# Optimization experiments

Measured on AMD Instinct MI355X. Metric: run time of the kernel, lower is better.

The kernel has to match this reference:

```python
import jax, jax.numpy as jnp
import numpy as np

FORGET_BIAS = 1.0  # TF BasicLSTMCell default

def _lstm_cell(c, h, x, W, b):
    # TF BasicLSTMCell: concat([x, h]) @ W + b, split into i, j(=g), f, o
    z = jnp.concatenate([x, h], axis=-1) @ W + b
    i, j, f, o = jnp.split(z, 4, axis=-1)
    c_new = c * jax.nn.sigmoid(f + FORGET_BIAS) + jax.nn.sigmoid(i) * jnp.tanh(j)
    h_new = jnp.tanh(c_new) * jax.nn.sigmoid(o)
    return c_new, h_new

def setup_inputs() -> dict:
    V, B, T, U = 16000, 64, 128, 256
    key = jax.random.key(0)
    ks = jax.random.split(key, 6)
    s_in = 1.0 / np.sqrt(2 * U)
    return {
        "input_data": jax.random.randint(ks[0], (B, T), 0, V, dtype=jnp.int32),
        "targets": jax.random.randint(ks[1], (B, T), 0, V, dtype=jnp.int32),
        "embedding": jax.random.normal(ks[2], (V, U), dtype=jnp.float32) * 0.1,
        "W0": jax.random.normal(ks[3], (2 * U, 4 * U), dtype=jnp.float32) * s_in,
        "b0": jnp.zeros((4 * U,), dtype=jnp.float32),
        "W1": jax.random.normal(ks[4], (2 * U, 4 * U), dtype=jnp.float32) * s_in,
        "b1": jnp.zeros((4 * U,), dtype=jnp.float32),
        "softmax_w": jax.random.normal(ks[5], (U, V), dtype=jnp.float32) * (1.0 / np.sqrt(U)),
        "softmax_b": jnp.zeros((V,), dtype=jnp.float32),
    }

def reference(input_data, targets, embedding, W0, b0, W1, b1, softmax_w, softmax_b):
    B, T = input_data.shape
    U = embedding.shape[1]
    # embedding lookup -> [B, T, U], scan over time (time-major)
    xs = embedding[input_data].transpose(1, 0, 2)  # [T, B, U]
    zeros = jnp.zeros((B, U), dtype=embedding.dtype)

    def step(carry, x):
        c0, h0, c1, h1 = carry
        c0, h0 = _lstm_cell(c0, h0, x, W0, b0)
        c1, h1 = _lstm_cell(c1, h1, h0, W1, b1)
        return (c0, h0, c1, h1), h1

    _, outs = jax.lax.scan(step, (zeros, zeros, zeros, zeros), xs)  # [T, B, U]
    output = outs.transpose(1, 0, 2).reshape(B * T, U)
    logits = output @ softmax_w + softmax_b  # [B*T, V]
    logp = jax.nn.log_softmax(logits, axis=-1)
    tgt = targets.reshape(-1)
    nll = -jnp.take_along_axis(logp, tgt[:, None], axis=-1)[:, 0]
    cost = jnp.sum(nll) / (B * T)
    return cost
```

## Files before the change

### kernel.cpp

```cpp
#include <hip/hip_runtime.h>
#include <hip/hip_bf16.h>
#include <stdint.h>

typedef __attribute__((ext_vector_type(8))) short short8;
typedef __attribute__((ext_vector_type(4))) float f32x4;
typedef unsigned long long u64;

#define DI static __device__ __forceinline__

DI unsigned short f2b(float f){
  unsigned u = __float_as_uint(f);
  u = (u + 0x7FFFu + ((u >> 16) & 1u)) >> 16;
  return (unsigned short)u;
}
DI float sigm(float x){ return 1.0f / (1.0f + __expf(-x)); }
DI float tanh_(float x){ return 1.0f - 2.0f / (__expf(2.0f*x) + 1.0f); }

__global__ void k_gather(const int* __restrict__ inp, const float* __restrict__ emb,
                         unsigned short* __restrict__ Xbf){
  int r = blockIdx.x;
  int t = r >> 6, b = r & 63;
  int idx = inp[b*128 + t];
  float v = emb[(size_t)idx*256 + threadIdx.x];
  Xbf[(size_t)r*256 + threadIdx.x] = f2b(v);
}

template<int BF, int REORD>
__global__ void k_transpose(const float* __restrict__ src, void* __restrict__ dst,
                            int R, int C, int ld, int row0){
  __shared__ float tile[32][33];
  int tx = threadIdx.x, ty = threadIdx.y;
  int x = blockIdx.x*32 + tx;
  for (int i = 0; i < 4; i++){
    int y = blockIdx.y*32 + ty + i*8;
    if (x < C && y < R) tile[ty + i*8][tx] = src[(size_t)(row0 + y)*ld + x];
  }
  __syncthreads();
  int y2 = blockIdx.y*32 + tx;
  for (int i = 0; i < 4; i++){
    int x2 = blockIdx.x*32 + ty + i*8;
    if (x2 < C && y2 < R){
      float v = tile[tx][ty + i*8];
      int n = REORD ? ((x2 & 255)*4 + (x2 >> 2 >> 6)) : x2;
      if (BF) ((unsigned short*)dst)[(size_t)n*R + y2] = f2b(v);
      else    ((float*)dst)[(size_t)n*R + y2] = v;
    }
  }
}

template<int EPI>
__launch_bounds__(256, 2)
__global__ void k_gemm(const unsigned short* __restrict__ A, const unsigned short* __restrict__ Bt,
                       float* __restrict__ outZ, const float* __restrict__ bias,
                       const int* __restrict__ tgt, float* __restrict__ S, float* __restrict__ LT){
  __shared__ unsigned short As[128*64];
  __shared__ unsigned short Bs[128*64];
  __shared__ int tgt_s[128];
  const int m0 = blockIdx.y*128, n0 = blockIdx.x*128;
  const int tid = threadIdx.x;
  const int w = tid >> 6, l = tid & 63;
  const int quad = l >> 4, l15 = l & 15;
  const int wm = (w >> 1)*64, wn = (w & 1)*64;
  const int lrow = l >> 3, ls = l & 7;
  f32x4 acc[4][4] = {};
  if (EPI == 1 && tid < 128) tgt_s[tid] = tgt[m0 + tid];

  for (int k0 = 0; k0 < 256; k0 += 64){
    #pragma unroll
    for (int it = 0; it < 4; it++){
      int row = it*32 + w*8 + lrow;
      int csrc = ls ^ (row & 7);
      __builtin_amdgcn_global_load_lds(
        (const __attribute__((address_space(1))) unsigned*)&A[(size_t)(m0+row)*256 + k0 + csrc*8],
        (__attribute__((address_space(3))) unsigned*)&As[(it*32 + w*8)*64], 16, 0, 0);
      __builtin_amdgcn_global_load_lds(
        (const __attribute__((address_space(1))) unsigned*)&Bt[(size_t)(n0+row)*256 + k0 + csrc*8],
        (__attribute__((address_space(3))) unsigned*)&Bs[(it*32 + w*8)*64], 16, 0, 0);
    }
    __syncthreads();
    #pragma unroll
    for (int ks = 0; ks < 64; ks += 32){
      const int cki = (ks >> 3) + quad;
      short8 af[4], bfr[4];
      #pragma unroll
      for (int i = 0; i < 4; i++){
        int row = wm + i*16 + l15;
        af[i]  = *(short8*)&As[row*64 + (cki ^ (row & 7))*8];
      }
      #pragma unroll
      for (int j = 0; j < 4; j++){
        int row = wn + j*16 + l15;
        bfr[j] = *(short8*)&Bs[row*64 + (cki ^ (row & 7))*8];
      }
      #pragma unroll
      for (int i = 0; i < 4; i++)
        #pragma unroll
        for (int j = 0; j < 4; j++)
          acc[i][j] = __builtin_amdgcn_mfma_f32_16x16x32_bf16(af[i], bfr[j], acc[i][j], 0, 0, 0);
    }
    __syncthreads();
  }

  if (EPI == 0){
    #pragma unroll
    for (int i = 0; i < 4; i++){
      int mg = m0 + wm + i*16 + quad*4;
      int t = mg >> 6, b = mg & 63;
      #pragma unroll
      for (int j = 0; j < 4; j++){
        int ng = n0 + wn + j*16 + l15;
        float bb = bias[(ng & 3)*256 + (ng >> 2)];
        f32x4 v = acc[i][j];
        v[0] += bb; v[1] += bb; v[2] += bb; v[3] += bb;
        *(f32x4*)&outZ[((size_t)t*1024 + ng)*64 + b] = v;
      }
    }
  } else {
    #pragma unroll
    for (int i = 0; i < 4; i++){
      float rs[4] = {0.f,0.f,0.f,0.f};
      #pragma unroll
      for (int j = 0; j < 4; j++){
        int ng = n0 + wn + j*16 + l15;
        float bb = bias[ng];
        f32x4 v = acc[i][j];
        #pragma unroll
        for (int r = 0; r < 4; r++){
          float e = v[r] + bb;
          int mloc = wm + i*16 + quad*4 + r;
          if (tgt_s[mloc] == ng) LT[m0 + mloc] = e;
          rs[r] += __expf(e);
        }
      }
      #pragma unroll
      for (int r = 0; r < 4; r++){
        float s = rs[r];
        s += __shfl_xor(s, 1, 16);
        s += __shfl_xor(s, 2, 16);
        s += __shfl_xor(s, 4, 16);
        s += __shfl_xor(s, 8, 16);
        if (l15 == 0) atomicAdd(&S[m0 + wm + i*16 + quad*4 + r], s);
      }
    }
  }
}

DI void stage32(const u64* __restrict__ src, unsigned* __restrict__ dst4, int tid, unsigned tagexp){
  u64 v[32];
  for (;;){
    bool ok = true;
    #pragma unroll
    for (int k = 0; k < 32; k++)
      v[k] = __hip_atomic_load(src + tid + k*256, __ATOMIC_RELAXED, __HIP_MEMORY_SCOPE_AGENT);
    #pragma unroll
    for (int k = 0; k < 32; k++)
      ok &= ((unsigned)(v[k] >> 32) == tagexp);
    if (ok) break;
    __builtin_amdgcn_s_sleep(1);
  }
  #pragma unroll
  for (int k = 0; k < 32; k++)
    dst4[tid + k*256] = (unsigned)v[k];
}

__launch_bounds__(256, 1)
__global__ void k_lstm(const float* __restrict__ Z0x,
                       const unsigned short* __restrict__ W0h,
                       const unsigned short* __restrict__ W1,
                       const float* __restrict__ b1,
                       u64* __restrict__ h0h,
                       u64* __restrict__ h1h,
                       unsigned short* __restrict__ H1bf){
  __shared__ __align__(16) char smraw[65536];
  unsigned short* hs = (unsigned short*)smraw;
  unsigned* hs4 = (unsigned*)smraw;
  float* zl = (float*)smraw;

  const int wg = blockIdx.x;
  const bool L0 = (wg < 8);
  const int tid = threadIdx.x;
  const int w = tid >> 6, l = tid & 63, quad = l >> 4, l15 = l & 15;
  const int b = tid & 63;

  short8 bw[16];
  float c_st[8];
  float b1r[16];
  #pragma unroll
  for (int i = 0; i < 8; i++) c_st[i] = 0.f;

  if (L0){
    const int n0 = wg*128;
    #pragma unroll
    for (int j = 0; j < 2; j++)
      #pragma unroll
      for (int ks = 0; ks < 8; ks++)
        bw[j*8+ks] = *(const short8*)&W0h[(size_t)(n0 + w*32 + j*16 + l15)*256 + ks*32 + quad*8];
  } else {
    const int n0 = (wg-8)*64;
    #pragma unroll
    for (int ks = 0; ks < 16; ks++)
      bw[ks] = *(const short8*)&W1[(size_t)(n0 + w*16 + l15)*512 + ks*32 + quad*8];
    const int u0 = (wg-8)*16, ul0 = w*4;
    #pragma unroll
    for (int ul = 0; ul < 4; ul++)
      #pragma unroll
      for (int g = 0; g < 4; g++)
        b1r[ul*4+g] = b1[g*256 + u0 + ul0 + ul];
  }

  if (L0){
    for (int t = 0; t < 128; t++){
      const int n0 = wg*128;
      f32x4 acc[4][2];
      #pragma unroll
      for (int i = 0; i < 4; i++)
        #pragma unroll
        for (int j = 0; j < 2; j++){
          int cl = w*32 + j*16 + l15;
          acc[i][j] = *(const f32x4*)&Z0x[((size_t)t*1024 + n0 + cl)*64 + i*16 + quad*4];
        }
      if (t > 0){
        stage32(h0h + (size_t)(t-1)*8192, hs4, tid, (unsigned)t);
        __syncthreads();
        #pragma unroll
        for (int ks = 0; ks < 8; ks++){
          short8 a[4];
          #pragma unroll
          for (int i = 0; i < 4; i++)
            a[i] = *(const short8*)&hs[(((ks*4+quad)*64) + i*16 + l15)*8];
          #pragma unroll
          for (int i = 0; i < 4; i++)
            #pragma unroll
            for (int j = 0; j < 2; j++)
              acc[i][j] = __builtin_amdgcn_mfma_f32_16x16x32_bf16(a[i], bw[j*8+ks], acc[i][j], 0, 0, 0);
        }
        __syncthreads();
      }
      #pragma unroll
      for (int i = 0; i < 4; i++)
        #pragma unroll
        for (int j = 0; j < 2; j++){
          int cl = w*32 + j*16 + l15;
          *(f32x4*)&zl[cl*68 + i*16 + quad*4] = acc[i][j];
        }
      __syncthreads();
      const int ul0 = w*8;
      unsigned short hout[8];
      #pragma unroll
      for (int ui = 0; ui < 8; ui++){
        int cc = (ul0 + ui)*4;
        float zi = zl[(cc+0)*68 + b], zj = zl[(cc+1)*68 + b];
        float zf = zl[(cc+2)*68 + b], zo = zl[(cc+3)*68 + b];
        float c = c_st[ui]*sigm(zf + 1.0f) + sigm(zi)*tanh_(zj);
        c_st[ui] = c;
        hout[ui] = f2b(tanh_(c)*sigm(zo));
      }
      const size_t base = (size_t)t*8192 + ((size_t)(wg*4 + w)*64 + b)*4;
      #pragma unroll
      for (int j = 0; j < 4; j++){
        u64 val = ((u64)(unsigned)(t+1) << 32)
                | (unsigned)hout[2*j] | ((unsigned)hout[2*j+1] << 16);
        __hip_atomic_store(h0h + base + j, val, __ATOMIC_RELAXED, __HIP_MEMORY_SCOPE_AGENT);
      }
      __syncthreads();
    }
  } else {
    for (int t = 0; t < 128; t++){
      stage32(h0h + (size_t)t*8192, hs4, tid, (unsigned)(t+1));
      __syncthreads();
      f32x4 acc[4];
      #pragma unroll
      for (int i = 0; i < 4; i++) acc[i] = (f32x4){0.f,0.f,0.f,0.f};
      #pragma unroll
      for (int ks = 0; ks < 8; ks++){
        short8 a[4];
        #pragma unroll
        for (int i = 0; i < 4; i++)
          a[i] = *(const short8*)&hs[(((ks*4+quad)*64) + i*16 + l15)*8];
        #pragma unroll
        for (int i = 0; i < 4; i++)
          acc[i] = __builtin_amdgcn_mfma_f32_16x16x32_bf16(a[i], bw[ks], acc[i], 0, 0, 0);
      }
      if (t > 0){
        stage32(h1h + (size_t)(t-1)*8192, hs4 + 8192, tid, (unsigned)t);
        __syncthreads();
        #pragma unroll
        for (int ks = 8; ks < 16; ks++){
          short8 a[4];
          #pragma unroll
          for (int i = 0; i < 4; i++)
            a[i] = *(const short8*)&hs[(((ks*4+quad)*64) + i*16 + l15)*8];
          #pragma unroll
          for (int i = 0; i < 4; i++)
            acc[i] = __builtin_amdgcn_mfma_f32_16x16x32_bf16(a[i], bw[ks], acc[i], 0, 0, 0);
        }
      }
      __syncthreads();
      {
        int cl = w*16 + l15;
        #pragma unroll
        for (int i = 0; i < 4; i++)
          *(f32x4*)&zl[cl*68 + i*16 + quad*4] = acc[i];
      }
      __syncthreads();
      const int u0 = (wg-8)*16, ul0 = w*4;
      unsigned short hout[4];
      #pragma unroll
      for (int ui = 0; ui < 4; ui++){
        int cc = (ul0 + ui)*4;
        float zi = zl[(cc+0)*68 + b] + b1r[ui*4+0];
        float zj = zl[(cc+1)*68 + b] + b1r[ui*4+1];
        float zf = zl[(cc+2)*68 + b] + b1r[ui*4+2];
        float zo = zl[(cc+3)*68 + b] + b1r[ui*4+3];
        float c = c_st[ui]*sigm(zf + 1.0f) + sigm(zi)*tanh_(zj);
        c_st[ui] = c;
        hout[ui] = f2b(tanh_(c)*sigm(zo));
      }
      const int u = u0 + ul0;
      const size_t base = (size_t)t*8192 + ((size_t)(u >> 3)*64 + b)*4 + ((u & 4) >> 1);
      #pragma unroll
      for (int j = 0; j < 2; j++){
        u64 val = ((u64)(unsigned)(t+1) << 32)
                | (unsigned)hout[2*j] | ((unsigned)hout[2*j+1] << 16);
        __hip_atomic_store(h1h + base + j, val, __ATOMIC_RELAXED, __HIP_MEMORY_SCOPE_AGENT);
      }
      *(uint2*)&H1bf[((size_t)b*128 + t)*256 + u] = *(const uint2*)hout;
      __syncthreads();
    }
  }
}

__global__ void k_reduce(const float* __restrict__ S, const float* __restrict__ LT,
                         float* __restrict__ out){
  __shared__ float red[256];
  float s = 0.f;
  for (int r = threadIdx.x; r < 8192; r += 256) s += __logf(S[r]) - LT[r];
  red[threadIdx.x] = s;
  __syncthreads();
  for (int st = 128; st > 0; st >>= 1){
    if (threadIdx.x < st) red[threadIdx.x] += red[threadIdx.x + st];
    __syncthreads();
  }
  if (threadIdx.x == 0) out[0] = red[0] / 8192.0f;
}

extern "C" void kernel_launch(void* const* d_in, const int* in_sizes, int n_in,
                              void* d_out, int out_size, void* d_ws, size_t ws_size,
                              hipStream_t stream){
  const int*   input   = (const int*)  d_in[0];
  const int*   targets = (const int*)  d_in[1];
  const float* emb     = (const float*)d_in[2];
  const float* W0      = (const float*)d_in[3];
  const float* b0      = (const float*)d_in[4];
  const float* W1      = (const float*)d_in[5];
  const float* b1      = (const float*)d_in[6];
  const float* Wsm     = (const float*)d_in[7];
  const float* sb      = (const float*)d_in[8];

  char* ws = (char*)d_ws;
  size_t off = 0;
  auto alloc = [&](size_t bytes)->char*{
    char* p = ws + off; off += (bytes + 255) & ~(size_t)255; return p;
  };
  unsigned short* Xbf  = (unsigned short*)alloc(8192ull*256*2);
  unsigned short* W0xT = (unsigned short*)alloc(1024ull*256*2);
  unsigned short* W0hT = (unsigned short*)alloc(1024ull*256*2);
  unsigned short* W1T  = (unsigned short*)alloc(1024ull*512*2);
  unsigned short* WsT  = (unsigned short*)alloc(16000ull*256*2);
  float*          Z0x  = (float*)         alloc(8192ull*1024*4);
  u64*            h0h  = (u64*)           alloc(128ull*8192*8);
  u64*            h1h  = (u64*)           alloc(128ull*8192*8);
  unsigned short* H1bf = (unsigned short*)alloc(8192ull*256*2);
  float*          S    = (float*)         alloc(8192ull*4);
  float*          LT   = (float*)         alloc(8192ull*4);

  hipMemsetAsync(S, 0, 8192ull*4, stream);

  k_gather<<<dim3(8192), dim3(256), 0, stream>>>(input, emb, Xbf);
  k_transpose<1,1><<<dim3(32, 8),  dim3(32,8), 0, stream>>>(W0,  (void*)W0xT, 256, 1024, 1024, 0);
  k_transpose<1,1><<<dim3(32, 8),  dim3(32,8), 0, stream>>>(W0,  (void*)W0hT, 256, 1024, 1024, 256);
  k_transpose<1,1><<<dim3(32, 16), dim3(32,8), 0, stream>>>(W1,  (void*)W1T,  512, 1024, 1024, 0);
  k_transpose<1,0><<<dim3(500, 8), dim3(32,8), 0, stream>>>(Wsm, (void*)WsT,  256, 16000, 16000, 0);

  k_gemm<0><<<dim3(8, 64), dim3(256), 0, stream>>>(Xbf, W0xT, Z0x, b0, nullptr, nullptr, nullptr);

  void* kargs[] = { (void*)&Z0x, (void*)&W0hT, (void*)&W1T, (void*)&b1,
                    (void*)&h0h, (void*)&h1h, (void*)&H1bf };
  hipLaunchCooperativeKernel((void*)k_lstm, dim3(24), dim3(256), kargs, 0, stream);

  k_gemm<1><<<dim3(125, 64), dim3(256), 0, stream>>>(H1bf, WsT, nullptr, sb, targets, S, LT);

  k_reduce<<<dim3(1), dim3(256), 0, stream>>>(S, LT, (float*)d_out);
}
```

Baseline: 1.043 ms.

## Restructure LSTM recurrence with per-wave gate ownership and canary flags

Each wave now computes all four gates for 16 units directly in MFMA registers, which removes the LDS round-trip of gate pre-activations. Layer 0 runs on 4 workgroups and layer 1 on 4, 8 in total instead of 24, so per-workgroup weight residency grows to 64 short8 registers. The per-element tagged 64-bit hidden-state handshake is replaced by bf16 stores that bypass to the last-level cache plus per-wave canary counters polled with a ballot, followed by direct global-to-LDS loads. The GEMM grid axes are also swapped and the weight transpose reordering dropped. In exchange, fewer CUs share the recurrent work and register pressure rises.

```diff
diff --git a/kernel.cpp b/kernel.cpp
--- a/kernel.cpp
+++ b/kernel.cpp
@@ -25,8 +25,7 @@
   Xbf[(size_t)r*256 + threadIdx.x] = f2b(v);
 }
 
-template<int BF, int REORD>
-__global__ void k_transpose(const float* __restrict__ src, void* __restrict__ dst,
+__global__ void k_transpose(const float* __restrict__ src, unsigned short* __restrict__ dst,
                             int R, int C, int ld, int row0){
   __shared__ float tile[32][33];
   int tx = threadIdx.x, ty = threadIdx.y;
@@ -39,12 +38,7 @@
   int y2 = blockIdx.y*32 + tx;
   for (int i = 0; i < 4; i++){
     int x2 = blockIdx.x*32 + ty + i*8;
-    if (x2 < C && y2 < R){
-      float v = tile[tx][ty + i*8];
-      int n = REORD ? ((x2 & 255)*4 + (x2 >> 2 >> 6)) : x2;
-      if (BF) ((unsigned short*)dst)[(size_t)n*R + y2] = f2b(v);
-      else    ((float*)dst)[(size_t)n*R + y2] = v;
-    }
+    if (x2 < C && y2 < R) dst[(size_t)x2*R + y2] = f2b(tile[tx][ty + i*8]);
   }
 }
 
@@ -56,7 +50,7 @@
   __shared__ unsigned short As[128*64];
   __shared__ unsigned short Bs[128*64];
   __shared__ int tgt_s[128];
-  const int m0 = blockIdx.y*128, n0 = blockIdx.x*128;
+  const int m0 = blockIdx.x*128, n0 = blockIdx.y*128;
   const int tid = threadIdx.x;
   const int w = tid >> 6, l = tid & 63;
   const int quad = l >> 4, l15 = l & 15;
@@ -109,7 +103,7 @@
       #pragma unroll
       for (int j = 0; j < 4; j++){
         int ng = n0 + wn + j*16 + l15;
-        float bb = bias[(ng & 3)*256 + (ng >> 2)];
+        float bb = bias[ng];
         f32x4 v = acc[i][j];
         v[0] += bb; v[1] += bb; v[2] += bb; v[3] += bb;
         *(f32x4*)&outZ[((size_t)t*1024 + ng)*64 + b] = v;
@@ -145,22 +139,16 @@
   }
 }
 
-DI void stage32(const u64* __restrict__ src, unsigned* __restrict__ dst4, int tid, unsigned tagexp){
-  u64 v[32];
-  for (;;){
-    bool ok = true;
-    #pragma unroll
-    for (int k = 0; k < 32; k++)
-      v[k] = __hip_atomic_load(src + tid + k*256, __ATOMIC_RELAXED, __HIP_MEMORY_SCOPE_AGENT);
-    #pragma unroll
-    for (int k = 0; k < 32; k++)
-      ok &= ((unsigned)(v[k] >> 32) == tagexp);
-    if (ok) break;
+DI void pollw(const unsigned* cz, int l, unsigned expv){
+  for(;;){
+    unsigned v = __hip_atomic_load(cz + (l & 15), __ATOMIC_RELAXED, __HIP_MEMORY_SCOPE_AGENT);
+    if (__ballot(v == expv) == ~0ull) break;
     __builtin_amdgcn_s_sleep(1);
   }
-  #pragma unroll
-  for (int k = 0; k < 32; k++)
-    dst4[tid + k*256] = (unsigned)v[k];
+  asm volatile("" ::: "memory");
+}
+DI void st_short_llc(unsigned short* p, unsigned v){
+  asm volatile("global_store_short %0, %1, off sc0 sc1" :: "v"(p), "v"(v) : "memory");
 }
 
 __launch_bounds__(256, 1)
@@ -168,164 +156,158 @@
                        const unsigned short* __restrict__ W0h,
                        const unsigned short* __restrict__ W1,
                        const float* __restrict__ b1,
-                       u64* __restrict__ h0h,
-                       u64* __restrict__ h1h,
-                       unsigned short* __restrict__ H1bf){
+                       unsigned short* __restrict__ h0h,
+                       unsigned short* __restrict__ h1h,
+                       unsigned short* __restrict__ H1bf,
+                       unsigned* __restrict__ canary0,
+                       unsigned* __restrict__ canary1){
   __shared__ __align__(16) char smraw[65536];
-  unsigned short* hs = (unsigned short*)smraw;
-  unsigned* hs4 = (unsigned*)smraw;
-  float* zl = (float*)smraw;
+  unsigned short* hs0 = (unsigned short*)smraw;
+  unsigned short* hs1 = (unsigned short*)(smraw + 32768);
 
   const int wg = blockIdx.x;
-  const bool L0 = (wg < 8);
+  const bool L0 = (wg < 4);
   const int tid = threadIdx.x;
   const int w = tid >> 6, l = tid & 63, quad = l >> 4, l15 = l & 15;
-  const int b = tid & 63;
-
-  short8 bw[16];
-  float c_st[8];
-  float b1r[16];
+
+  float c_st[16];
   #pragma unroll
-  for (int i = 0; i < 8; i++) c_st[i] = 0.f;
+  for (int i = 0; i < 16; i++) c_st[i] = 0.f;
 
   if (L0){
-    const int n0 = wg*128;
-    #pragma unroll
-    for (int j = 0; j < 2; j++)
+    const int gw = wg*4 + w;
+    const int u0 = gw*16;
+    short8 bw[32];
+    #pragma unroll
+    for (int g = 0; g < 4; g++)
       #pragma unroll
       for (int ks = 0; ks < 8; ks++)
-        bw[j*8+ks] = *(const short8*)&W0h[(size_t)(n0 + w*32 + j*16 + l15)*256 + ks*32 + quad*8];
-  } else {
-    const int n0 = (wg-8)*64;
-    #pragma unroll
-    for (int ks = 0; ks < 16; ks++)
-      bw[ks] = *(const short8*)&W1[(size_t)(n0 + w*16 + l15)*512 + ks*32 + quad*8];
-    const int u0 = (wg-8)*16, ul0 = w*4;
-    #pragma unroll
-    for (int ul = 0; ul < 4; ul++)
-      #pragma unroll
-      for (int g = 0; g < 4; g++)
-        b1r[ul*4+g] = b1[g*256 + u0 + ul0 + ul];
-  }
-
-  if (L0){
+        bw[g*8+ks] = *(const short8*)&W0h[(size_t)(g*256 + u0 + l15)*256 + ks*32 + quad*8];
+
     for (int t = 0; t < 128; t++){
-      const int n0 = wg*128;
-      f32x4 acc[4][2];
+      f32x4 acc[4][4];
       #pragma unroll
       for (int i = 0; i < 4; i++)
         #pragma unroll
-        for (int j = 0; j < 2; j++){
-          int cl = w*32 + j*16 + l15;
-          acc[i][j] = *(const f32x4*)&Z0x[((size_t)t*1024 + n0 + cl)*64 + i*16 + quad*4];
-        }
+        for (int g = 0; g < 4; g++)
+          acc[i][g] = *(const f32x4*)&Z0x[((size_t)t*1024 + g*256 + u0 + l15)*64 + i*16 + quad*4];
       if (t > 0){
-        stage32(h0h + (size_t)(t-1)*8192, hs4, tid, (unsigned)t);
+        __syncthreads();
+        pollw(canary0 + (t-1)*16, l, (unsigned)t);
+        #pragma unroll
+        for (int it = 0; it < 8; it++){
+          int c = it*256 + w*64 + l;
+          __builtin_amdgcn_global_load_lds(
+            (const __attribute__((address_space(1))) unsigned*)&h0h[((size_t)(t-1)*2048 + c)*8],
+            (__attribute__((address_space(3))) unsigned*)&hs0[(size_t)(it*256 + w*64)*8], 16, 0, 0);
+        }
         __syncthreads();
         #pragma unroll
         for (int ks = 0; ks < 8; ks++){
           short8 a[4];
           #pragma unroll
           for (int i = 0; i < 4; i++)
-            a[i] = *(const short8*)&hs[(((ks*4+quad)*64) + i*16 + l15)*8];
+            a[i] = *(const short8*)&hs0[(((ks*4+quad)*64) + i*16 + l15)*8];
           #pragma unroll
           for (int i = 0; i < 4; i++)
             #pragma unroll
-            for (int j = 0; j < 2; j++)
-              acc[i][j] = __builtin_amdgcn_mfma_f32_16x16x32_bf16(a[i], bw[j*8+ks], acc[i][j], 0, 0, 0);
-        }
+            for (int g = 0; g < 4; g++)
+              acc[i][g] = __builtin_amdgcn_mfma_f32_16x16x32_bf16(a[i], bw[g*8+ks], acc[i][g], 0, 0, 0);
+        }
+      }
+      const int kb = (u0 >> 3) + (l15 >> 3), pos = l15 & 7;
+      #pragma unroll
+      for (int i = 0; i < 4; i++)
+        #pragma unroll
+        for (int r = 0; r < 4; r++){
+          float zi = acc[i][0][r], zj = acc[i][1][r], zf = acc[i][2][r], zo = acc[i][3][r];
+          float c = c_st[i*4+r]*sigm(zf + 1.0f) + sigm(zi)*tanh_(zj);
+          c_st[i*4+r] = c;
+          unsigned short hv = f2b(tanh_(c)*sigm(zo));
+          int b = i*16 + quad*4 + r;
+          st_short_llc(h0h + ((size_t)t*2048 + (size_t)kb*64 + b)*8 + pos, (unsigned)hv);
+        }
+      asm volatile("s_waitcnt vmcnt(0)" ::: "memory");
+      if (l == 0)
+        __hip_atomic_store(canary0 + t*16 + gw, (unsigned)(t+1), __ATOMIC_RELAXED, __HIP_MEMORY_SCOPE_AGENT);
+    }
+  } else {
+    const int gw = (wg-4)*4 + w;
+    const int u0 = gw*16;
+    short8 bw[64];
+    #pragma unroll
+    for (int g = 0; g < 4; g++)
+      #pragma unroll
+      for (int ks = 0; ks < 16; ks++)
+        bw[g*16+ks] = *(const short8*)&W1[(size_t)(g*256 + u0 + l15)*512 + ks*32 + quad*8];
+    float b1r[4];
+    #pragma unroll
+    for (int g = 0; g < 4; g++) b1r[g] = b1[g*256 + u0 + l15];
+
+    for (int t = 0; t < 128; t++){
+      f32x4 acc[4][4] = {};
+      if (t > 0){
         __syncthreads();
-      }
-      #pragma unroll
-      for (int i = 0; i < 4; i++)
-        #pragma unroll
-        for (int j = 0; j < 2; j++){
-          int cl = w*32 + j*16 + l15;
-          *(f32x4*)&zl[cl*68 + i*16 + quad*4] = acc[i][j];
-        }
+        pollw(canary1 + (t-1)*16, l, (unsigned)t);
+        #pragma unroll
+        for (int it = 0; it < 8; it++){
+          int c = it*256 + w*64 + l;
+          __builtin_amdgcn_global_load_lds(
+            (const __attribute__((address_space(1))) unsigned*)&h1h[((size_t)(t-1)*2048 + c)*8],
+            (__attribute__((address_space(3))) unsigned*)&hs1[(size_t)(it*256 + w*64)*8], 16, 0, 0);
+        }
+        __syncthreads();
+        #pragma unroll
+        for (int ks = 8; ks < 16; ks++){
+          short8 a[4];
+          #pragma unroll
+          for (int i = 0; i < 4; i++)
+            a[i] = *(const short8*)&hs1[((((ks-8)*4+quad)*64) + i*16 + l15)*8];
+          #pragma unroll
+          for (int i = 0; i < 4; i++)
+            #pragma unroll
+            for (int g = 0; g < 4; g++)
+              acc[i][g] = __builtin_amdgcn_mfma_f32_16x16x32_bf16(a[i], bw[g*16+ks], acc[i][g], 0, 0, 0);
+        }
+      }
+      pollw(canary0 + t*16, l, (unsigned)(t+1));
+      #pragma unroll
+      for (int it = 0; it < 8; it++){
+        int c = it*256 + w*64 + l;
+        __builtin_amdgcn_global_load_lds(
+          (const __attribute__((address_space(1))) unsigned*)&h0h[((size_t)t*2048 + c)*8],
+          (__attribute__((address_space(3))) unsigned*)&hs0[(size_t)(it*256 + w*64)*8], 16, 0, 0);
+      }
       __syncthreads();
-      const int ul0 = w*8;
-      unsigned short hout[8];
-      #pragma unroll
-      for (int ui = 0; ui < 8; ui++){
-        int cc = (ul0 + ui)*4;
-        float zi = zl[(cc+0)*68 + b], zj = zl[(cc+1)*68 + b];
-        float zf = zl[(cc+2)*68 + b], zo = zl[(cc+3)*68 + b];
-        float c = c_st[ui]*sigm(zf + 1.0f) + sigm(zi)*tanh_(zj);
-        c_st[ui] = c;
-        hout[ui] = f2b(tanh_(c)*sigm(zo));
-      }
-      const size_t base = (size_t)t*8192 + ((size_t)(wg*4 + w)*64 + b)*4;
-      #pragma unroll
-      for (int j = 0; j < 4; j++){
-        u64 val = ((u64)(unsigned)(t+1) << 32)
-                | (unsigned)hout[2*j] | ((unsigned)hout[2*j+1] << 16);
-        __hip_atomic_store(h0h + base + j, val, __ATOMIC_RELAXED, __HIP_MEMORY_SCOPE_AGENT);
-      }
-      __syncthreads();
-    }
-  } else {
-    for (int t = 0; t < 128; t++){
-      stage32(h0h + (size_t)t*8192, hs4, tid, (unsigned)(t+1));
-      __syncthreads();
-      f32x4 acc[4];
-      #pragma unroll
-      for (int i = 0; i < 4; i++) acc[i] = (f32x4){0.f,0.f,0.f,0.f};
       #pragma unroll
       for (int ks = 0; ks < 8; ks++){
         short8 a[4];
         #pragma unroll
         for (int i = 0; i < 4; i++)
-          a[i] = *(const short8*)&hs[(((ks*4+quad)*64) + i*16 + l15)*8];
+          a[i] = *(const short8*)&hs0[(((ks*4+quad)*64) + i*16 + l15)*8];
         #pragma unroll
         for (int i = 0; i < 4; i++)
-          acc[i] = __builtin_amdgcn_mfma_f32_16x16x32_bf16(a[i], bw[ks], acc[i], 0, 0, 0);
-      }
-      if (t > 0){
-        stage32(h1h + (size_t)(t-1)*8192, hs4 + 8192, tid, (unsigned)t);
-        __syncthreads();
-        #pragma unroll
-        for (int ks = 8; ks < 16; ks++){
-          short8 a[4];
-          #pragma unroll
-          for (int i = 0; i < 4; i++)
-            a[i] = *(const short8*)&hs[(((ks*4+quad)*64) + i*16 + l15)*8];
-          #pragma unroll
-          for (int i = 0; i < 4; i++)
-            acc[i] = __builtin_amdgcn_mfma_f32_16x16x32_bf16(a[i], bw[ks], acc[i], 0, 0, 0);
-        }
-      }
-      __syncthreads();
-      {
-        int cl = w*16 + l15;
-        #pragma unroll
-        for (int i = 0; i < 4; i++)
-          *(f32x4*)&zl[cl*68 + i*16 + quad*4] = acc[i];
-      }
-      __syncthreads();
-      const int u0 = (wg-8)*16, ul0 = w*4;
-      unsigned short hout[4];
-      #pragma unroll
-      for (int ui = 0; ui < 4; ui++){
-        int cc = (ul0 + ui)*4;
-        float zi = zl[(cc+0)*68 + b] + b1r[ui*4+0];
-        float zj = zl[(cc+1)*68 + b] + b1r[ui*4+1];
-        float zf = zl[(cc+2)*68 + b] + b1r[ui*4+2];
-        float zo = zl[(cc+3)*68 + b] + b1r[ui*4+3];
-        float c = c_st[ui]*sigm(zf + 1.0f) + sigm(zi)*tanh_(zj);
-        c_st[ui] = c;
-        hout[ui] = f2b(tanh_(c)*sigm(zo));
-      }
-      const int u = u0 + ul0;
-      const size_t base = (size_t)t*8192 + ((size_t)(u >> 3)*64 + b)*4 + ((u & 4) >> 1);
-      #pragma unroll
-      for (int j = 0; j < 2; j++){
-        u64 val = ((u64)(unsigned)(t+1) << 32)
-                | (unsigned)hout[2*j] | ((unsigned)hout[2*j+1] << 16);
-        __hip_atomic_store(h1h + base + j, val, __ATOMIC_RELAXED, __HIP_MEMORY_SCOPE_AGENT);
-      }
-      *(uint2*)&H1bf[((size_t)b*128 + t)*256 + u] = *(const uint2*)hout;
-      __syncthreads();
+          #pragma unroll
+          for (int g = 0; g < 4; g++)
+            acc[i][g] = __builtin_amdgcn_mfma_f32_16x16x32_bf16(a[i], bw[g*16+ks], acc[i][g], 0, 0, 0);
+      }
+      const int kb = (u0 >> 3) + (l15 >> 3), pos = l15 & 7;
+      #pragma unroll
+      for (int i = 0; i < 4; i++)
+        #pragma unroll
+        for (int r = 0; r < 4; r++){
+          float zi = acc[i][0][r] + b1r[0], zj = acc[i][1][r] + b1r[1];
+          float zf = acc[i][2][r] + b1r[2], zo = acc[i][3][r] + b1r[3];
+          float c = c_st[i*4+r]*sigm(zf + 1.0f) + sigm(zi)*tanh_(zj);
+          c_st[i*4+r] = c;
+          unsigned short hv = f2b(tanh_(c)*sigm(zo));
+          int b = i*16 + quad*4 + r;
+          st_short_llc(h1h + ((size_t)t*2048 + (size_t)kb*64 + b)*8 + pos, (unsigned)hv);
+          H1bf[((size_t)b*128 + t)*256 + u0 + l15] = hv;
+        }
+      asm volatile("s_waitcnt vmcnt(0)" ::: "memory");
+      if (l == 0)
+        __hip_atomic_store(canary1 + t*16 + gw, (unsigned)(t+1), __ATOMIC_RELAXED, __HIP_MEMORY_SCOPE_AGENT);
     }
   }
 }
@@ -368,27 +350,30 @@
   unsigned short* W1T  = (unsigned short*)alloc(1024ull*512*2);
   unsigned short* WsT  = (unsigned short*)alloc(16000ull*256*2);
   float*          Z0x  = (float*)         alloc(8192ull*1024*4);
-  u64*            h0h  = (u64*)           alloc(128ull*8192*8);
-  u64*            h1h  = (u64*)           alloc(128ull*8192*8);
+  unsigned short* h0h  = (unsigned short*)alloc(128ull*2048*16);
+  unsigned short* h1h  = (unsigned short*)alloc(128ull*2048*16);
   unsigned short* H1bf = (unsigned short*)alloc(8192ull*256*2);
   float*          S    = (float*)         alloc(8192ull*4);
   float*          LT   = (float*)         alloc(8192ull*4);
+  unsigned*       canary0 = (unsigned*)   alloc(128*16*4);
+  unsigned*       canary1 = (unsigned*)   alloc(128*16*4);
 
   hipMemsetAsync(S, 0, 8192ull*4, stream);
+  hipMemsetAsync(canary0, 0, 2*128*16*4, stream);
 
   k_gather<<<dim3(8192), dim3(256), 0, stream>>>(input, emb, Xbf);
-  k_transpose<1,1><<<dim3(32, 8),  dim3(32,8), 0, stream>>>(W0,  (void*)W0xT, 256, 1024, 1024, 0);
-  k_transpose<1,1><<<dim3(32, 8),  dim3(32,8), 0, stream>>>(W0,  (void*)W0hT, 256, 1024, 1024, 256);
-  k_transpose<1,1><<<dim3(32, 16), dim3(32,8), 0, stream>>>(W1,  (void*)W1T,  512, 1024, 1024, 0);
-  k_transpose<1,0><<<dim3(500, 8), dim3(32,8), 0, stream>>>(Wsm, (void*)WsT,  256, 16000, 16000, 0);
-
-  k_gemm<0><<<dim3(8, 64), dim3(256), 0, stream>>>(Xbf, W0xT, Z0x, b0, nullptr, nullptr, nullptr);
+  k_transpose<<<dim3(32, 8),  dim3(32,8), 0, stream>>>(W0,  W0xT, 256, 1024, 1024, 0);
+  k_transpose<<<dim3(32, 8),  dim3(32,8), 0, stream>>>(W0,  W0hT, 256, 1024, 1024, 256);
+  k_transpose<<<dim3(32, 16), dim3(32,8), 0, stream>>>(W1,  W1T,  512, 1024, 1024, 0);
+  k_transpose<<<dim3(500, 8), dim3(32,8), 0, stream>>>(Wsm, WsT,  256, 16000, 16000, 0);
+
+  k_gemm<0><<<dim3(64, 8), dim3(256), 0, stream>>>(Xbf, W0xT, Z0x, b0, nullptr, nullptr, nullptr);
 
   void* kargs[] = { (void*)&Z0x, (void*)&W0hT, (void*)&W1T, (void*)&b1,
-                    (void*)&h0h, (void*)&h1h, (void*)&H1bf };
-  hipLaunchCooperativeKernel((void*)k_lstm, dim3(24), dim3(256), kargs, 0, stream);
-
-  k_gemm<1><<<dim3(125, 64), dim3(256), 0, stream>>>(H1bf, WsT, nullptr, sb, targets, S, LT);
+                    (void*)&h0h, (void*)&h1h, (void*)&H1bf, (void*)&canary0, (void*)&canary1 };
+  hipLaunchCooperativeKernel((void*)k_lstm, dim3(8), dim3(256), kargs, 0, stream);
+
+  k_gemm<1><<<dim3(64, 125), dim3(256), 0, stream>>>(H1bf, WsT, nullptr, sb, targets, S, LT);
 
   k_reduce<<<dim3(1), dim3(256), 0, stream>>>(S, LT, (float*)d_out);
 }
```

Result: slower. 1.323 ms (+26.9%).
